# Kernel optimization log

Measured on AMD Instinct MI355X. Metric: run time of the kernel, lower is better.

The kernel has to match this reference:

```python
import jax, jax.numpy as jnp
import numpy as np

N_QUBITS = 6
N_LAYERS = 8
N_CLASSES = 4
BATCH = 262144
DIM = 2 ** N_QUBITS  # 64


def setup_inputs() -> dict:
    key = jax.random.key(0)
    k1, k2, k3, k4 = jax.random.split(key, 4)
    x = jax.random.normal(k1, (BATCH, DIM), dtype=jnp.float32)
    # TorchLayer default init for StronglyEntanglingLayers weights: U(0, 2*pi)
    weights = jax.random.uniform(k2, (N_LAYERS, N_QUBITS, 3), dtype=jnp.float32,
                                 minval=0.0, maxval=2.0 * np.pi)
    fc_w = jax.random.normal(k3, (N_CLASSES, N_QUBITS), dtype=jnp.float32) * 0.3
    fc_b = jax.random.normal(k4, (N_CLASSES,), dtype=jnp.float32) * 0.1
    return {"x": x, "weights": weights, "fc_w": fc_w, "fc_b": fc_b}


def _rot_mats(weights):
    # PennyLane Rot(phi, theta, omega) = RZ(omega) RY(theta) RZ(phi)
    phi, theta, omega = weights[..., 0], weights[..., 1], weights[..., 2]
    c = jnp.cos(theta / 2)
    s = jnp.sin(theta / 2)
    m00 = jnp.exp(-0.5j * (phi + omega)) * c
    m01 = -jnp.exp(0.5j * (phi - omega)) * s
    m10 = jnp.exp(-0.5j * (phi - omega)) * s
    m11 = jnp.exp(0.5j * (phi + omega)) * c
    # [L, n, 2, 2] complex64
    return jnp.stack([jnp.stack([m00, m01], -1), jnp.stack([m10, m11], -1)], -2).astype(jnp.complex64)


def _apply_1q(state, U, q):
    # state: [B, 2, 2, 2, 2, 2, 2]; apply 2x2 gate U on qubit axis q+1
    ax = q + 1
    s = jnp.moveaxis(state, ax, -1)
    s = jnp.einsum('ij,...j->...i', U, s)
    return jnp.moveaxis(s, -1, ax)


def _cnot(state, c, t):
    # flip target qubit t on the control==1 slice of qubit c
    axc = c + 1
    s0 = jax.lax.index_in_dim(state, 0, axis=axc, keepdims=False)
    s1 = jax.lax.index_in_dim(state, 1, axis=axc, keepdims=False)
    t_ax = t + 1 if t < c else t  # target axis after removing control axis
    s1 = jnp.flip(s1, axis=t_ax)
    return jnp.stack([s0, s1], axis=axc)


def _pauli_z_signs():
    # qubit 0 is the most significant bit of the basis-state index
    bits = (jnp.arange(DIM)[:, None] >> jnp.arange(N_QUBITS - 1, -1, -1)[None, :]) & 1
    return (1 - 2 * bits).astype(jnp.float32)  # [DIM, N_QUBITS]


def reference(x, weights, fc_w, fc_b):
    B = x.shape[0]
    # F.normalize(p=2) + AmplitudeEmbedding(normalize=True) -> single L2 normalize
    xn = x / jnp.maximum(jnp.linalg.norm(x, axis=1, keepdims=True), 1e-12)
    state = xn.astype(jnp.complex64).reshape((B,) + (2,) * N_QUBITS)
    U = _rot_mats(weights)  # [L, n, 2, 2]
    for l in range(N_LAYERS):
        for q in range(N_QUBITS):
            state = _apply_1q(state, U[l, q], q)
        r = (l % (N_QUBITS - 1)) + 1  # StronglyEntanglingLayers default ranges
        for q in range(N_QUBITS):
            state = _cnot(state, q, (q + r) % N_QUBITS)
    probs = (state.real ** 2 + state.imag ** 2).reshape(B, DIM)
    expvals = probs @ _pauli_z_signs()  # [B, n] <Z_i>
    return expvals @ fc_w.T + fc_b
```

## Files before the change

### kernel.cpp

```cpp
#include <hip/hip_runtime.h>

#define NQ 6
#define DIM 64
#define NL 8

#define KP  136
#define ROWS 128

typedef __attribute__((ext_vector_type(8))) short    short8v;
typedef __attribute__((ext_vector_type(4))) float    floatx4;
typedef __attribute__((ext_vector_type(4))) _Float16 half4v;

__device__ inline short f2bf_rne(float f) {
    unsigned u = __float_as_uint(f);
    u += 0x7FFF + ((u >> 16) & 1);
    return (short)(u >> 16);
}

__global__ __launch_bounds__(64) void qnn_prep(
    const float* __restrict__ wts,
    const float* __restrict__ fc_w,
    void* __restrict__ ws)
{
    __shared__ float gc[48][4];
    const int n   = threadIdx.x;
    const int col = blockIdx.x;

    if (n < 48) {
        float phi = wts[n*3+0], th = wts[n*3+1], om = wts[n*3+2];
        float ch = cosf(0.5f*th), sh = sinf(0.5f*th);
        float p  = 0.5f*(phi+om), m  = 0.5f*(phi-om);
        gc[n][0] = cosf(p)*ch;
        gc[n][1] = sinf(p)*ch;
        gc[n][2] = cosf(m)*sh;
        gc[n][3] = sinf(m)*sh;
    }
    __syncthreads();

    float ar = (n == col) ? 1.0f : 0.0f;
    float ai = 0.0f;

    #pragma unroll
    for (int l = 0; l < NL; ++l) {
        #pragma unroll
        for (int q = 0; q < NQ; ++q) {
            const int g     = l*NQ + q;
            const int shift = 5 - q;
            const int mask  = 1 << shift;
            const int b     = (n >> shift) & 1;
            const float cpch = gc[g][0];
            const float spch = gc[g][1];
            const float cmsh = gc[g][2];
            const float smsh = gc[g][3];
            const float pr = __shfl_xor(ar, mask, 64);
            const float pi = __shfl_xor(ai, mask, 64);
            const float udr = cpch;
            const float udi = b ?  spch : -spch;
            const float uor = b ?  cmsh : -cmsh;
            const float uoi = -smsh;
            const float nr = udr*ar - udi*ai + uor*pr - uoi*pi;
            const float ni = udr*ai + udi*ar + uor*pi + uoi*pr;
            ar = nr; ai = ni;
        }
        const int r = (l % (NQ - 1)) + 1;
        #pragma unroll
        for (int q = 0; q < NQ; ++q) {
            const int t     = (q + r) % NQ;
            const int cmask = 1 << (5 - q);
            const int tmask = 1 << (5 - t);
            const float pr = __shfl_xor(ar, tmask, 64);
            const float pi = __shfl_xor(ai, tmask, 64);
            const bool ctrl = (n & cmask) != 0;
            ar = ctrl ? pr : ar;
            ai = ctrl ? pi : ai;
        }
    }

    unsigned short* Bs = (unsigned short*)ws;
    unsigned short hr = (unsigned short)f2bf_rne(ar);
    float hrf = __uint_as_float((unsigned)hr << 16);
    unsigned short lr = (unsigned short)f2bf_rne(ar - hrf);
    unsigned short hi = (unsigned short)f2bf_rne(ai);
    float hif = __uint_as_float((unsigned)hi << 16);
    unsigned short li = (unsigned short)f2bf_rne(ai - hif);
    Bs[n*KP + col]           = hr;
    Bs[n*KP + 64 + col]      = lr;
    Bs[(64+n)*KP + col]      = hi;
    Bs[(64+n)*KP + 64 + col] = li;

    if (col == 0) {
        const int cp = n & 15;
        const int qd = n >> 4;
        half4v* Mo = (half4v*)((char*)ws + 128*KP*2);
        #pragma unroll
        for (int c2 = 0; c2 < 4; ++c2) {
            half4v h4;
            #pragma unroll
            for (int j = 0; j < 4; ++j) {
                const int i = c2*16 + qd*4 + j;
                float v = 0.f;
                if (cp < 4) {
                    #pragma unroll
                    for (int q = 0; q < NQ; ++q) {
                        const float sgn = 1.0f - 2.0f*(float)((i >> (5-q)) & 1);
                        v = fmaf(sgn, fc_w[cp*NQ + q], v);
                    }
                } else if (cp == 4) {
                    v = 1.0f;
                }
                h4[j] = (_Float16)v;
            }
            Mo[c2*64 + n] = h4;
        }
    }
}

__global__ __launch_bounds__(256, 2) void qnn_main(
    const float* __restrict__ x,
    const float* __restrict__ fc_b,
    const void* __restrict__ wsv,
    float* __restrict__ out)
{
    __shared__ __align__(16) unsigned short Bs[128*KP];

    const int tid  = threadIdx.x;
    const int s0   = blockIdx.x * ROWS;
    const int lane = tid & 63;
    const int w    = tid >> 6;
    const int l15  = lane & 15;
    const int quad = lane >> 4;

    {
        const floatx4* bg = (const floatx4*)wsv;
        floatx4* bl = (floatx4*)Bs;
        #pragma unroll
        for (int i = 0; i < 9; ++i) {
            int idx = tid + i*256;
            if (idx < 128*KP*2/16) bl[idx] = bg[idx];
        }
    }

    short8v xf[2][2];
    #pragma unroll
    for (int st = 0; st < 2; ++st) {
        const size_t row = (size_t)(s0 + w*32 + st*16 + l15);
        const float* xp = x + row*DIM + quad*8;
        #pragma unroll
        for (int h = 0; h < 2; ++h) {
            float4 u0 = *(const float4*)(xp + h*32);
            float4 u1 = *(const float4*)(xp + h*32 + 4);
            short8v a;
            a[0]=f2bf_rne(u0.x); a[1]=f2bf_rne(u0.y);
            a[2]=f2bf_rne(u0.z); a[3]=f2bf_rne(u0.w);
            a[4]=f2bf_rne(u1.x); a[5]=f2bf_rne(u1.y);
            a[6]=f2bf_rne(u1.z); a[7]=f2bf_rne(u1.w);
            xf[st][h] = a;
        }
    }
    __syncthreads();

    floatx4 acc[2][8];
    #pragma unroll
    for (int st = 0; st < 2; ++st)
        #pragma unroll
        for (int mt = 0; mt < 8; ++mt)
            acc[st][mt] = (floatx4){0.f, 0.f, 0.f, 0.f};

    #pragma unroll
    for (int kk = 0; kk < 4; ++kk) {
        const int h  = kk & 1;
        const int bk = (kk << 5) + quad*8;
        short8v wf[8];
        #pragma unroll
        for (int mt = 0; mt < 8; ++mt)
            wf[mt] = *(const short8v*)&Bs[(mt*16 + l15)*KP + bk];
        #pragma unroll
        for (int mt = 0; mt < 8; ++mt) {
            acc[0][mt] = __builtin_amdgcn_mfma_f32_16x16x32_bf16(wf[mt], xf[0][h], acc[0][mt], 0, 0, 0);
            acc[1][mt] = __builtin_amdgcn_mfma_f32_16x16x32_bf16(wf[mt], xf[1][h], acc[1][mt], 0, 0, 0);
        }
    }

    const half4v* Mg = (const half4v*)((const char*)wsv + 128*KP*2);
    half4v a2[4];
    #pragma unroll
    for (int c2 = 0; c2 < 4; ++c2) a2[c2] = Mg[c2*64 + lane];

    const float b0 = fc_b[0], b1 = fc_b[1], b2 = fc_b[2], b3 = fc_b[3];

    #pragma unroll
    for (int st = 0; st < 2; ++st) {
        floatx4 d2 = (floatx4){0.f, 0.f, 0.f, 0.f};
        #pragma unroll
        for (int c2 = 0; c2 < 4; ++c2) {
            half4v pb;
            #pragma unroll
            for (int r = 0; r < 4; ++r) {
                const float re = acc[st][c2][r];
                const float im = acc[st][c2 + 4][r];
                pb[r] = (_Float16)fmaf(re, re, im*im);
            }
            d2 = __builtin_amdgcn_mfma_f32_16x16x16f16(a2[c2], pb, d2, 0, 0, 0);
        }
        const float ssv = __shfl_xor(d2[0], 16, 64);
        if (quad == 0) {
            const float inv = 1.0f / ssv;
            float4 o;
            o.x = fmaf(d2[0], inv, b0);
            o.y = fmaf(d2[1], inv, b1);
            o.z = fmaf(d2[2], inv, b2);
            o.w = fmaf(d2[3], inv, b3);
            *(float4*)(out + (size_t)(s0 + w*32 + st*16 + l15)*4) = o;
        }
    }
}

extern "C" void kernel_launch(void* const* d_in, const int* in_sizes, int n_in,
                              void* d_out, int out_size, void* d_ws, size_t ws_size,
                              hipStream_t stream) {
    const float* x    = (const float*)d_in[0];
    const float* wts  = (const float*)d_in[1];
    const float* fc_w = (const float*)d_in[2];
    const float* fc_b = (const float*)d_in[3];
    float* out = (float*)d_out;

    const int batch = in_sizes[0] / DIM;

    qnn_prep<<<DIM, DIM, 0, stream>>>(wts, fc_w, d_ws);
    qnn_main<<<batch / ROWS, 256, 0, stream>>>(x, fc_b, d_ws, out);
}
```

Measured before the change: 109.3 us.

## Make main kernel process multiple tiles per block with register-prefetched x

```diff
diff --git a/kernel.cpp b/kernel.cpp
--- a/kernel.cpp
+++ b/kernel.cpp
@@ -4,8 +4,9 @@
 #define DIM 64
 #define NL 8
 
-#define KP  136
+#define KP   136
 #define ROWS 128
+#define TPB  4
 
 typedef __attribute__((ext_vector_type(8))) short    short8v;
 typedef __attribute__((ext_vector_type(4))) float    floatx4;
@@ -124,11 +125,24 @@
     __shared__ __align__(16) unsigned short Bs[128*KP];
 
     const int tid  = threadIdx.x;
-    const int s0   = blockIdx.x * ROWS;
     const int lane = tid & 63;
     const int w    = tid >> 6;
     const int l15  = lane & 15;
     const int quad = lane >> 4;
+    const int nb   = gridDim.x;
+    const int rbase = w*32 + l15;
+
+    float4 xr[2][2][2][2];
+    {
+        const float* xt = x + ((size_t)blockIdx.x*ROWS + rbase)*DIM + quad*8;
+        #pragma unroll
+        for (int st = 0; st < 2; ++st)
+            #pragma unroll
+            for (int h = 0; h < 2; ++h) {
+                xr[0][st][h][0] = *(const float4*)(xt + st*16*DIM + h*32);
+                xr[0][st][h][1] = *(const float4*)(xt + st*16*DIM + h*32 + 4);
+            }
+    }
 
     {
         const floatx4* bg = (const floatx4*)wsv;
@@ -137,47 +151,6 @@
         for (int i = 0; i < 9; ++i) {
             int idx = tid + i*256;
             if (idx < 128*KP*2/16) bl[idx] = bg[idx];
-        }
-    }
-
-    short8v xf[2][2];
-    #pragma unroll
-    for (int st = 0; st < 2; ++st) {
-        const size_t row = (size_t)(s0 + w*32 + st*16 + l15);
-        const float* xp = x + row*DIM + quad*8;
-        #pragma unroll
-        for (int h = 0; h < 2; ++h) {
-            float4 u0 = *(const float4*)(xp + h*32);
-            float4 u1 = *(const float4*)(xp + h*32 + 4);
-            short8v a;
-            a[0]=f2bf_rne(u0.x); a[1]=f2bf_rne(u0.y);
-            a[2]=f2bf_rne(u0.z); a[3]=f2bf_rne(u0.w);
-            a[4]=f2bf_rne(u1.x); a[5]=f2bf_rne(u1.y);
-            a[6]=f2bf_rne(u1.z); a[7]=f2bf_rne(u1.w);
-            xf[st][h] = a;
-        }
-    }
-    __syncthreads();
-
-    floatx4 acc[2][8];
-    #pragma unroll
-    for (int st = 0; st < 2; ++st)
-        #pragma unroll
-        for (int mt = 0; mt < 8; ++mt)
-            acc[st][mt] = (floatx4){0.f, 0.f, 0.f, 0.f};
-
-    #pragma unroll
-    for (int kk = 0; kk < 4; ++kk) {
-        const int h  = kk & 1;
-        const int bk = (kk << 5) + quad*8;
-        short8v wf[8];
-        #pragma unroll
-        for (int mt = 0; mt < 8; ++mt)
-            wf[mt] = *(const short8v*)&Bs[(mt*16 + l15)*KP + bk];
-        #pragma unroll
-        for (int mt = 0; mt < 8; ++mt) {
-            acc[0][mt] = __builtin_amdgcn_mfma_f32_16x16x32_bf16(wf[mt], xf[0][h], acc[0][mt], 0, 0, 0);
-            acc[1][mt] = __builtin_amdgcn_mfma_f32_16x16x32_bf16(wf[mt], xf[1][h], acc[1][mt], 0, 0, 0);
         }
     }
 
@@ -188,29 +161,83 @@
 
     const float b0 = fc_b[0], b1 = fc_b[1], b2 = fc_b[2], b3 = fc_b[3];
 
+    __syncthreads();
+
     #pragma unroll
-    for (int st = 0; st < 2; ++st) {
-        floatx4 d2 = (floatx4){0.f, 0.f, 0.f, 0.f};
-        #pragma unroll
-        for (int c2 = 0; c2 < 4; ++c2) {
-            half4v pb;
-            #pragma unroll
-            for (int r = 0; r < 4; ++r) {
-                const float re = acc[st][c2][r];
-                const float im = acc[st][c2 + 4][r];
-                pb[r] = (_Float16)fmaf(re, re, im*im);
-            }
-            d2 = __builtin_amdgcn_mfma_f32_16x16x16f16(a2[c2], pb, d2, 0, 0, 0);
-        }
-        const float ssv = __shfl_xor(d2[0], 16, 64);
-        if (quad == 0) {
-            const float inv = 1.0f / ssv;
-            float4 o;
-            o.x = fmaf(d2[0], inv, b0);
-            o.y = fmaf(d2[1], inv, b1);
-            o.z = fmaf(d2[2], inv, b2);
-            o.w = fmaf(d2[3], inv, b3);
-            *(float4*)(out + (size_t)(s0 + w*32 + st*16 + l15)*4) = o;
+    for (int t = 0; t < TPB; ++t) {
+        const int buf = t & 1;
+
+        if (t < TPB - 1) {
+            const size_t tile1 = (size_t)(blockIdx.x + (t+1)*nb);
+            const float* xt = x + (tile1*ROWS + rbase)*DIM + quad*8;
+            #pragma unroll
+            for (int st = 0; st < 2; ++st)
+                #pragma unroll
+                for (int h = 0; h < 2; ++h) {
+                    xr[buf^1][st][h][0] = *(const float4*)(xt + st*16*DIM + h*32);
+                    xr[buf^1][st][h][1] = *(const float4*)(xt + st*16*DIM + h*32 + 4);
+                }
+        }
+
+        short8v xf[2][2];
+        #pragma unroll
+        for (int st = 0; st < 2; ++st)
+            #pragma unroll
+            for (int h = 0; h < 2; ++h) {
+                const float4 u0 = xr[buf][st][h][0];
+                const float4 u1 = xr[buf][st][h][1];
+                short8v a;
+                a[0]=f2bf_rne(u0.x); a[1]=f2bf_rne(u0.y);
+                a[2]=f2bf_rne(u0.z); a[3]=f2bf_rne(u0.w);
+                a[4]=f2bf_rne(u1.x); a[5]=f2bf_rne(u1.y);
+                a[6]=f2bf_rne(u1.z); a[7]=f2bf_rne(u1.w);
+                xf[st][h] = a;
+            }
+
+        floatx4 acc[2][8];
+        #pragma unroll
+        for (int st = 0; st < 2; ++st)
+            #pragma unroll
+            for (int mt = 0; mt < 8; ++mt)
+                acc[st][mt] = (floatx4){0.f, 0.f, 0.f, 0.f};
+
+        #pragma unroll
+        for (int kk = 0; kk < 4; ++kk) {
+            const int h  = kk & 1;
+            const int bk = (kk << 5) + quad*8;
+            #pragma unroll
+            for (int mt = 0; mt < 8; ++mt) {
+                const short8v wf = *(const short8v*)&Bs[(mt*16 + l15)*KP + bk];
+                acc[0][mt] = __builtin_amdgcn_mfma_f32_16x16x32_bf16(wf, xf[0][h], acc[0][mt], 0, 0, 0);
+                acc[1][mt] = __builtin_amdgcn_mfma_f32_16x16x32_bf16(wf, xf[1][h], acc[1][mt], 0, 0, 0);
+            }
+        }
+
+        const size_t s0 = (size_t)(blockIdx.x + t*nb) * ROWS;
+        #pragma unroll
+        for (int st = 0; st < 2; ++st) {
+            floatx4 d2 = (floatx4){0.f, 0.f, 0.f, 0.f};
+            #pragma unroll
+            for (int c2 = 0; c2 < 4; ++c2) {
+                half4v pb;
+                #pragma unroll
+                for (int r = 0; r < 4; ++r) {
+                    const float re = acc[st][c2][r];
+                    const float im = acc[st][c2 + 4][r];
+                    pb[r] = (_Float16)fmaf(re, re, im*im);
+                }
+                d2 = __builtin_amdgcn_mfma_f32_16x16x16f16(a2[c2], pb, d2, 0, 0, 0);
+            }
+            const float ssv = __shfl_xor(d2[0], 16, 64);
+            if (quad == 0) {
+                const float inv = 1.0f / ssv;
+                float4 o;
+                o.x = fmaf(d2[0], inv, b0);
+                o.y = fmaf(d2[1], inv, b1);
+                o.z = fmaf(d2[2], inv, b2);
+                o.w = fmaf(d2[3], inv, b3);
+                *(float4*)(out + (s0 + w*32 + st*16 + l15)*4) = o;
+            }
         }
     }
 }
@@ -227,5 +254,5 @@
     const int batch = in_sizes[0] / DIM;
 
     qnn_prep<<<DIM, DIM, 0, stream>>>(wts, fc_w, d_ws);
-    qnn_main<<<batch / ROWS, 256, 0, stream>>>(x, fc_b, d_ws, out);
-}
+    qnn_main<<<batch / (ROWS*TPB), 256, 0, stream>>>(x, fc_b, d_ws, out);
+}
```

Result: no change. 107.2 us (-1.9%).

## Make main kernel persistent with register-resident weights and double-buffered x loads

Applied to the files above, without the earlier changes.

```diff
diff --git a/kernel.cpp b/kernel.cpp
--- a/kernel.cpp
+++ b/kernel.cpp
@@ -5,7 +5,7 @@
 #define NL 8
 
 #define KP  136
-#define ROWS 128
+#define TPW 8
 
 typedef __attribute__((ext_vector_type(8))) short    short8v;
 typedef __attribute__((ext_vector_type(4))) float    floatx4;
@@ -76,17 +76,17 @@
         }
     }
 
-    unsigned short* Bs = (unsigned short*)ws;
+    unsigned short* Bw = (unsigned short*)ws;
     unsigned short hr = (unsigned short)f2bf_rne(ar);
     float hrf = __uint_as_float((unsigned)hr << 16);
     unsigned short lr = (unsigned short)f2bf_rne(ar - hrf);
     unsigned short hi = (unsigned short)f2bf_rne(ai);
     float hif = __uint_as_float((unsigned)hi << 16);
     unsigned short li = (unsigned short)f2bf_rne(ai - hif);
-    Bs[n*KP + col]           = hr;
-    Bs[n*KP + 64 + col]      = lr;
-    Bs[(64+n)*KP + col]      = hi;
-    Bs[(64+n)*KP + 64 + col] = li;
+    Bw[n*KP + col]           = hr;
+    Bw[n*KP + 64 + col]      = lr;
+    Bw[(64+n)*KP + col]      = hi;
+    Bw[(64+n)*KP + 64 + col] = li;
 
     if (col == 0) {
         const int cp = n & 15;
@@ -121,65 +121,20 @@
     const void* __restrict__ wsv,
     float* __restrict__ out)
 {
-    __shared__ __align__(16) unsigned short Bs[128*KP];
-
     const int tid  = threadIdx.x;
-    const int s0   = blockIdx.x * ROWS;
     const int lane = tid & 63;
     const int w    = tid >> 6;
     const int l15  = lane & 15;
     const int quad = lane >> 4;
-
-    {
-        const floatx4* bg = (const floatx4*)wsv;
-        floatx4* bl = (floatx4*)Bs;
-        #pragma unroll
-        for (int i = 0; i < 9; ++i) {
-            int idx = tid + i*256;
-            if (idx < 128*KP*2/16) bl[idx] = bg[idx];
-        }
-    }
-
-    short8v xf[2][2];
+    const size_t gw = (size_t)blockIdx.x*4 + w;
+
+    const unsigned short* Wb = (const unsigned short*)wsv;
+    short8v wfr[4][8];
     #pragma unroll
-    for (int st = 0; st < 2; ++st) {
-        const size_t row = (size_t)(s0 + w*32 + st*16 + l15);
-        const float* xp = x + row*DIM + quad*8;
-        #pragma unroll
-        for (int h = 0; h < 2; ++h) {
-            float4 u0 = *(const float4*)(xp + h*32);
-            float4 u1 = *(const float4*)(xp + h*32 + 4);
-            short8v a;
-            a[0]=f2bf_rne(u0.x); a[1]=f2bf_rne(u0.y);
-            a[2]=f2bf_rne(u0.z); a[3]=f2bf_rne(u0.w);
-            a[4]=f2bf_rne(u1.x); a[5]=f2bf_rne(u1.y);
-            a[6]=f2bf_rne(u1.z); a[7]=f2bf_rne(u1.w);
-            xf[st][h] = a;
-        }
-    }
-    __syncthreads();
-
-    floatx4 acc[2][8];
-    #pragma unroll
-    for (int st = 0; st < 2; ++st)
+    for (int kk = 0; kk < 4; ++kk)
         #pragma unroll
         for (int mt = 0; mt < 8; ++mt)
-            acc[st][mt] = (floatx4){0.f, 0.f, 0.f, 0.f};
-
-    #pragma unroll
-    for (int kk = 0; kk < 4; ++kk) {
-        const int h  = kk & 1;
-        const int bk = (kk << 5) + quad*8;
-        short8v wf[8];
-        #pragma unroll
-        for (int mt = 0; mt < 8; ++mt)
-            wf[mt] = *(const short8v*)&Bs[(mt*16 + l15)*KP + bk];
-        #pragma unroll
-        for (int mt = 0; mt < 8; ++mt) {
-            acc[0][mt] = __builtin_amdgcn_mfma_f32_16x16x32_bf16(wf[mt], xf[0][h], acc[0][mt], 0, 0, 0);
-            acc[1][mt] = __builtin_amdgcn_mfma_f32_16x16x32_bf16(wf[mt], xf[1][h], acc[1][mt], 0, 0, 0);
-        }
-    }
+            wfr[kk][mt] = *(const short8v*)(Wb + (mt*16 + l15)*KP + kk*32 + quad*8);
 
     const half4v* Mg = (const half4v*)((const char*)wsv + 128*KP*2);
     half4v a2[4];
@@ -188,31 +143,85 @@
 
     const float b0 = fc_b[0], b1 = fc_b[1], b2 = fc_b[2], b3 = fc_b[3];
 
-    #pragma unroll
-    for (int st = 0; st < 2; ++st) {
-        floatx4 d2 = (floatx4){0.f, 0.f, 0.f, 0.f};
-        #pragma unroll
-        for (int c2 = 0; c2 < 4; ++c2) {
-            half4v pb;
-            #pragma unroll
-            for (int r = 0; r < 4; ++r) {
-                const float re = acc[st][c2][r];
-                const float im = acc[st][c2 + 4][r];
-                pb[r] = (_Float16)fmaf(re, re, im*im);
-            }
-            d2 = __builtin_amdgcn_mfma_f32_16x16x16f16(a2[c2], pb, d2, 0, 0, 0);
-        }
-        const float ssv = __shfl_xor(d2[0], 16, 64);
-        if (quad == 0) {
-            const float inv = 1.0f / ssv;
-            float4 o;
-            o.x = fmaf(d2[0], inv, b0);
-            o.y = fmaf(d2[1], inv, b1);
-            o.z = fmaf(d2[2], inv, b2);
-            o.w = fmaf(d2[3], inv, b3);
-            *(float4*)(out + (size_t)(s0 + w*32 + st*16 + l15)*4) = o;
-        }
-    }
+    const float* xbase = x + (gw*TPW*16 + (size_t)l15)*DIM + quad*8;
+
+    float4 xr[2][4];
+
+    xr[0][0] = *(const float4*)(xbase);
+    xr[0][1] = *(const float4*)(xbase + 4);
+    xr[0][2] = *(const float4*)(xbase + 32);
+    xr[0][3] = *(const float4*)(xbase + 36);
+
+#define QNN_COMPUTE(BUF, TI)                                                   \
+    {                                                                          \
+        short8v xf[2];                                                         \
+        _Pragma("unroll")                                                      \
+        for (int h = 0; h < 2; ++h) {                                          \
+            const float4 u0 = xr[BUF][2*h];                                    \
+            const float4 u1 = xr[BUF][2*h + 1];                                \
+            short8v a;                                                         \
+            a[0]=f2bf_rne(u0.x); a[1]=f2bf_rne(u0.y);                          \
+            a[2]=f2bf_rne(u0.z); a[3]=f2bf_rne(u0.w);                          \
+            a[4]=f2bf_rne(u1.x); a[5]=f2bf_rne(u1.y);                          \
+            a[6]=f2bf_rne(u1.z); a[7]=f2bf_rne(u1.w);                          \
+            xf[h] = a;                                                         \
+        }                                                                      \
+        floatx4 acc[8];                                                        \
+        _Pragma("unroll")                                                      \
+        for (int mt = 0; mt < 8; ++mt) acc[mt] = (floatx4){0.f,0.f,0.f,0.f};   \
+        _Pragma("unroll")                                                      \
+        for (int kk = 0; kk < 4; ++kk) {                                       \
+            const int h = kk & 1;                                              \
+            _Pragma("unroll")                                                  \
+            for (int mt = 0; mt < 8; ++mt)                                     \
+                acc[mt] = __builtin_amdgcn_mfma_f32_16x16x32_bf16(             \
+                    wfr[kk][mt], xf[h], acc[mt], 0, 0, 0);                     \
+        }                                                                      \
+        floatx4 d2 = (floatx4){0.f,0.f,0.f,0.f};                               \
+        _Pragma("unroll")                                                      \
+        for (int c2 = 0; c2 < 4; ++c2) {                                       \
+            half4v pb;                                                         \
+            _Pragma("unroll")                                                  \
+            for (int r = 0; r < 4; ++r) {                                      \
+                const float re = acc[c2][r];                                   \
+                const float im = acc[c2 + 4][r];                               \
+                pb[r] = (_Float16)fmaf(re, re, im*im);                         \
+            }                                                                  \
+            d2 = __builtin_amdgcn_mfma_f32_16x16x16f16(a2[c2], pb, d2, 0,0,0); \
+        }                                                                      \
+        const float ssv = __shfl_xor(d2[0], 16, 64);                           \
+        if (quad == 0) {                                                       \
+            const float inv = 1.0f / ssv;                                      \
+            float4 o;                                                          \
+            o.x = fmaf(d2[0], inv, b0);                                        \
+            o.y = fmaf(d2[1], inv, b1);                                        \
+            o.z = fmaf(d2[2], inv, b2);                                        \
+            o.w = fmaf(d2[3], inv, b3);                                        \
+            *(float4*)(out + (gw*TPW + (TI))*16*4 + (size_t)l15*4) = o;        \
+        }                                                                      \
+    }
+
+    #pragma clang loop unroll(disable)
+    for (int t = 0; t < TPW; t += 2) {
+        {
+            const float* xt = xbase + (size_t)(t + 1) * 1024;
+            xr[1][0] = *(const float4*)(xt);
+            xr[1][1] = *(const float4*)(xt + 4);
+            xr[1][2] = *(const float4*)(xt + 32);
+            xr[1][3] = *(const float4*)(xt + 36);
+        }
+        QNN_COMPUTE(0, t)
+        {
+            const int tn = (t + 2 < TPW) ? (t + 2) : (TPW - 1);
+            const float* xt = xbase + (size_t)tn * 1024;
+            xr[0][0] = *(const float4*)(xt);
+            xr[0][1] = *(const float4*)(xt + 4);
+            xr[0][2] = *(const float4*)(xt + 32);
+            xr[0][3] = *(const float4*)(xt + 36);
+        }
+        QNN_COMPUTE(1, t + 1)
+    }
+#undef QNN_COMPUTE
 }
 
 extern "C" void kernel_launch(void* const* d_in, const int* in_sizes, int n_in,
@@ -224,8 +233,6 @@
     const float* fc_b = (const float*)d_in[3];
     float* out = (float*)d_out;
 
-    const int batch = in_sizes[0] / DIM;
-
     qnn_prep<<<DIM, DIM, 0, stream>>>(wts, fc_w, d_ws);
-    qnn_main<<<batch / ROWS, 256, 0, stream>>>(x, fc_b, d_ws, out);
-}
+    qnn_main<<<512, 256, 0, stream>>>(x, fc_b, d_ws, out);
+}
```

Measured after the change: 110.4 us. About the same (+1.0%).

## Switch unitary matmul to single fp16 MFMA and shrink LDS for higher occupancy

Applied to the files above, without the earlier changes.

```diff
diff --git a/kernel.cpp b/kernel.cpp
--- a/kernel.cpp
+++ b/kernel.cpp
@@ -4,18 +4,10 @@
 #define DIM 64
 #define NL 8
 
-#define KP  136
-#define ROWS 128
-
-typedef __attribute__((ext_vector_type(8))) short    short8v;
+#define WP  72
+
 typedef __attribute__((ext_vector_type(4))) float    floatx4;
 typedef __attribute__((ext_vector_type(4))) _Float16 half4v;
-
-__device__ inline short f2bf_rne(float f) {
-    unsigned u = __float_as_uint(f);
-    u += 0x7FFF + ((u >> 16) & 1);
-    return (short)(u >> 16);
-}
 
 __global__ __launch_bounds__(64) void qnn_prep(
     const float* __restrict__ wts,
@@ -76,22 +68,14 @@
         }
     }
 
-    unsigned short* Bs = (unsigned short*)ws;
-    unsigned short hr = (unsigned short)f2bf_rne(ar);
-    float hrf = __uint_as_float((unsigned)hr << 16);
-    unsigned short lr = (unsigned short)f2bf_rne(ar - hrf);
-    unsigned short hi = (unsigned short)f2bf_rne(ai);
-    float hif = __uint_as_float((unsigned)hi << 16);
-    unsigned short li = (unsigned short)f2bf_rne(ai - hif);
-    Bs[n*KP + col]           = hr;
-    Bs[n*KP + 64 + col]      = lr;
-    Bs[(64+n)*KP + col]      = hi;
-    Bs[(64+n)*KP + 64 + col] = li;
+    _Float16* Wf = (_Float16*)ws;
+    Wf[n*WP + col]      = (_Float16)ar;
+    Wf[(64+n)*WP + col] = (_Float16)ai;
 
     if (col == 0) {
         const int cp = n & 15;
         const int qd = n >> 4;
-        half4v* Mo = (half4v*)((char*)ws + 128*KP*2);
+        half4v* Mo = (half4v*)((char*)ws + 128*WP*2);
         #pragma unroll
         for (int c2 = 0; c2 < 4; ++c2) {
             half4v h4;
@@ -115,89 +99,83 @@
     }
 }
 
-__global__ __launch_bounds__(256, 2) void qnn_main(
+__global__ __launch_bounds__(256, 4) void qnn_main(
     const float* __restrict__ x,
     const float* __restrict__ fc_b,
     const void* __restrict__ wsv,
     float* __restrict__ out)
 {
-    __shared__ __align__(16) unsigned short Bs[128*KP];
+    __shared__ __align__(16) _Float16 Ws[128*WP];
 
     const int tid  = threadIdx.x;
-    const int s0   = blockIdx.x * ROWS;
     const int lane = tid & 63;
     const int w    = tid >> 6;
     const int l15  = lane & 15;
     const int quad = lane >> 4;
+    const size_t gw = (size_t)blockIdx.x*4 + w;
+
+    float4 xr[2][4];
+    #pragma unroll
+    for (int t = 0; t < 2; ++t) {
+        const float* xp = x + (gw*32 + (size_t)t*16 + l15)*DIM + quad*4;
+        #pragma unroll
+        for (int kc = 0; kc < 4; ++kc)
+            xr[t][kc] = *(const float4*)(xp + kc*16);
+    }
 
     {
-        const floatx4* bg = (const floatx4*)wsv;
-        floatx4* bl = (floatx4*)Bs;
-        #pragma unroll
-        for (int i = 0; i < 9; ++i) {
-            int idx = tid + i*256;
-            if (idx < 128*KP*2/16) bl[idx] = bg[idx];
-        }
-    }
-
-    short8v xf[2][2];
-    #pragma unroll
-    for (int st = 0; st < 2; ++st) {
-        const size_t row = (size_t)(s0 + w*32 + st*16 + l15);
-        const float* xp = x + row*DIM + quad*8;
-        #pragma unroll
-        for (int h = 0; h < 2; ++h) {
-            float4 u0 = *(const float4*)(xp + h*32);
-            float4 u1 = *(const float4*)(xp + h*32 + 4);
-            short8v a;
-            a[0]=f2bf_rne(u0.x); a[1]=f2bf_rne(u0.y);
-            a[2]=f2bf_rne(u0.z); a[3]=f2bf_rne(u0.w);
-            a[4]=f2bf_rne(u1.x); a[5]=f2bf_rne(u1.y);
-            a[6]=f2bf_rne(u1.z); a[7]=f2bf_rne(u1.w);
-            xf[st][h] = a;
-        }
-    }
+        const floatx4* wg = (const floatx4*)wsv;
+        floatx4* wl = (floatx4*)Ws;
+        #pragma unroll
+        for (int i = 0; i < 5; ++i) {
+            const int idx = tid + i*256;
+            if (idx < 128*WP*2/16) wl[idx] = wg[idx];
+        }
+    }
+
+    const half4v* Mg = (const half4v*)((const char*)wsv + 128*WP*2);
+    half4v a2[4];
+    #pragma unroll
+    for (int c2 = 0; c2 < 4; ++c2) a2[c2] = Mg[c2*64 + lane];
+    const float b0 = fc_b[0], b1 = fc_b[1], b2 = fc_b[2], b3 = fc_b[3];
+
     __syncthreads();
 
-    floatx4 acc[2][8];
-    #pragma unroll
-    for (int st = 0; st < 2; ++st)
-        #pragma unroll
-        for (int mt = 0; mt < 8; ++mt)
-            acc[st][mt] = (floatx4){0.f, 0.f, 0.f, 0.f};
-
-    #pragma unroll
-    for (int kk = 0; kk < 4; ++kk) {
-        const int h  = kk & 1;
-        const int bk = (kk << 5) + quad*8;
-        short8v wf[8];
-        #pragma unroll
-        for (int mt = 0; mt < 8; ++mt)
-            wf[mt] = *(const short8v*)&Bs[(mt*16 + l15)*KP + bk];
-        #pragma unroll
-        for (int mt = 0; mt < 8; ++mt) {
-            acc[0][mt] = __builtin_amdgcn_mfma_f32_16x16x32_bf16(wf[mt], xf[0][h], acc[0][mt], 0, 0, 0);
-            acc[1][mt] = __builtin_amdgcn_mfma_f32_16x16x32_bf16(wf[mt], xf[1][h], acc[1][mt], 0, 0, 0);
-        }
-    }
-
-    const half4v* Mg = (const half4v*)((const char*)wsv + 128*KP*2);
-    half4v a2[4];
-    #pragma unroll
-    for (int c2 = 0; c2 < 4; ++c2) a2[c2] = Mg[c2*64 + lane];
-
-    const float b0 = fc_b[0], b1 = fc_b[1], b2 = fc_b[2], b3 = fc_b[3];
-
-    #pragma unroll
-    for (int st = 0; st < 2; ++st) {
+    #pragma unroll
+    for (int t = 0; t < 2; ++t) {
+        half4v xf[4];
+        #pragma unroll
+        for (int kc = 0; kc < 4; ++kc) {
+            const float4 u = xr[t][kc];
+            half4v h;
+            h[0] = (_Float16)u.x; h[1] = (_Float16)u.y;
+            h[2] = (_Float16)u.z; h[3] = (_Float16)u.w;
+            xf[kc] = h;
+        }
+
+        floatx4 acc[8];
+        #pragma unroll
+        for (int mt = 0; mt < 8; ++mt) acc[mt] = (floatx4){0.f, 0.f, 0.f, 0.f};
+
+        #pragma unroll
+        for (int kc = 0; kc < 4; ++kc) {
+            #pragma unroll
+            for (int mt = 0; mt < 8; ++mt) {
+                const half4v wf = *(const half4v*)
+                    &Ws[(mt*16 + l15)*WP + kc*16 + quad*4];
+                acc[mt] = __builtin_amdgcn_mfma_f32_16x16x16f16(
+                    wf, xf[kc], acc[mt], 0, 0, 0);
+            }
+        }
+
         floatx4 d2 = (floatx4){0.f, 0.f, 0.f, 0.f};
         #pragma unroll
         for (int c2 = 0; c2 < 4; ++c2) {
             half4v pb;
             #pragma unroll
             for (int r = 0; r < 4; ++r) {
-                const float re = acc[st][c2][r];
-                const float im = acc[st][c2 + 4][r];
+                const float re = acc[c2][r];
+                const float im = acc[c2 + 4][r];
                 pb[r] = (_Float16)fmaf(re, re, im*im);
             }
             d2 = __builtin_amdgcn_mfma_f32_16x16x16f16(a2[c2], pb, d2, 0, 0, 0);
@@ -210,7 +188,7 @@
             o.y = fmaf(d2[1], inv, b1);
             o.z = fmaf(d2[2], inv, b2);
             o.w = fmaf(d2[3], inv, b3);
-            *(float4*)(out + (size_t)(s0 + w*32 + st*16 + l15)*4) = o;
+            *(float4*)(out + (gw*32 + (size_t)t*16 + l15)*4) = o;
         }
     }
 }
@@ -224,8 +202,6 @@
     const float* fc_b = (const float*)d_in[3];
     float* out = (float*)d_out;
 
-    const int batch = in_sizes[0] / DIM;
-
     qnn_prep<<<DIM, DIM, 0, stream>>>(wts, fc_w, d_ws);
-    qnn_main<<<batch / ROWS, 256, 0, stream>>>(x, fc_b, d_ws, out);
+    qnn_main<<<2048, 256, 0, stream>>>(x, fc_b, d_ws, out);
 }
```

After: 108.9 us. About the same (-0.3%).
